# Optimization experiments

Hardware: AMD Instinct MI355X
Metric: run time of the kernel (lower is better)

## Reference

```python
import jax, jax.numpy as jnp
import numpy as np

DIM = 64
D_STATE = 64          # = d_inner // 2, required for consistency
D_CONV = 4
EXPAND = 2
D_INNER = EXPAND * DIM  # 128
BATCH = 2
SEQ = 2048


def setup_inputs() -> dict:
    key = jax.random.key(0)
    k0, k1, k2, k3, k4, k5 = jax.random.split(key, 6)
    return {
        "x": jax.random.normal(k0, (BATCH, SEQ, DIM), jnp.float32),
        # torch nn.Linear weight layout: (out_features, in_features)
        "W_proj": jax.random.normal(k1, (3 * D_INNER, DIM), jnp.float32) / np.sqrt(DIM),
        # torch depthwise Conv1d weight layout: (d_inner, 1, d_conv)
        "conv_w": jax.random.normal(k2, (D_INNER, 1, D_CONV), jnp.float32) / np.sqrt(D_CONV),
        "conv_b": jax.random.normal(k3, (D_INNER,), jnp.float32) * 0.01,
        # negative A so exp(delta * rowsum(A)) is a stable decay (<1)
        "A": -jnp.abs(jax.random.normal(k4, (D_STATE, D_STATE), jnp.float32)) * 0.1,
        "D": jax.random.normal(k5, (D_INNER,), jnp.float32),
    }


def _scan_dir(A_bar, bx, reverse):
    # A_bar, bx: (B, L, n, d). Linear recurrence h_t = A_t * h_{t-1} + bx_t.
    A_t = jnp.moveaxis(A_bar, 1, 0)  # (L, B, n, d)
    b_t = jnp.moveaxis(bx, 1, 0)
    h0 = jnp.zeros(A_t.shape[1:], A_t.dtype)

    def step(h, inp):
        a, b = inp
        h = a * h + b
        return h, h

    _, hs = jax.lax.scan(step, h0, (A_t, b_t), reverse=reverse)
    return jnp.moveaxis(hs, 0, 1)  # (B, L, n, d)


def _forward(x, W_proj, conv_w, conv_b, A, D):
    d_inner = D.shape[0]
    n = A.shape[0]
    k = conv_w.shape[-1]

    xp = x @ W_proj.T                                   # (B, L, 3*d_inner)
    x_c_in, delta_raw, BC = jnp.split(xp, [d_inner, 2 * d_inner], axis=-1)

    # causal depthwise conv1d (torch pads d_conv-1 both sides then slices [:L])
    xc = jnp.swapaxes(x_c_in, 1, 2)                     # (B, d, L)
    xc = jax.lax.conv_general_dilated(
        xc, conv_w, window_strides=(1,), padding=[(k - 1, 0)],
        dimension_numbers=("NCH", "OIH", "NCH"), feature_group_count=d_inner)
    xc = xc + conv_b[None, :, None]
    x_conv = jnp.swapaxes(xc, 1, 2)                     # (B, L, d_inner)

    delta = jax.nn.sigmoid(delta_raw)                   # (B, L, d_inner)
    B_in, C_in = BC[..., :n], BC[..., n:]               # (B, L, n) each

    a = A.sum(axis=1)                                   # 'ij->i' contraction, (n,)
    # A_bar[b,l,n,d] = exp(delta[b,l,d] * a[n])
    A_bar = jnp.exp(delta[:, :, None, :] * a[None, None, :, None])
    # (delta*B) * x, broadcast into (B, L, n, d)
    bx = (delta * x_conv)[:, :, None, :] * B_in[..., None]

    h = _scan_dir(A_bar, bx, False) + _scan_dir(A_bar, bx, True)  # (B,L,n,d)

    y = jnp.einsum("blnd,bln->bld", h, C_in) + D * x_conv
    return y


def reference(x, W_proj, conv_w, conv_b, A, D):
    return _forward(x, W_proj, conv_w, conv_b, A, D)
```

## Files before the change

kernel.cpp:

```cpp
#include <hip/hip_runtime.h>

#define BB   2
#define TT   2048
#define DIN  128
#define NS   64
#define CL   16
#define NC   128
#define NSUP 16
#define SUPW 8
#define NP   32
#define L2E  1.4426950408889634f

typedef float f2_t __attribute__((ext_vector_type(2)));
typedef float f4_t __attribute__((ext_vector_type(4)));

#if __has_builtin(__builtin_amdgcn_exp2f)
__device__ __forceinline__ float fexp2(float x) { return __builtin_amdgcn_exp2f(x); }
#else
__device__ __forceinline__ float fexp2(float x) { return exp2f(x); }
#endif

__device__ __forceinline__ unsigned int f2bfu(float f) {
  unsigned int u = __float_as_uint(f);
  u += 0x7FFFu + ((u >> 16) & 1u);
  return u >> 16;
}
__device__ __forceinline__ unsigned int packbf2(float a, float b) {
  return f2bfu(a) | (f2bfu(b) << 16);
}
__device__ __forceinline__ float bflo(unsigned int u) { return __uint_as_float(u << 16); }
__device__ __forceinline__ float bfhi(unsigned int u) { return __uint_as_float(u & 0xFFFF0000u); }

__global__ __launch_bounds__(128) void k_proj(
    const float* __restrict__ x, const float* __restrict__ W,
    const float* __restrict__ A,
    float* __restrict__ xcin, float* __restrict__ delta,
    float* __restrict__ Bb, float* __restrict__ Cb, float* __restrict__ a2g) {
  __shared__ float xs[128 * 65];
  int tile = blockIdx.x, rg = blockIdx.y, tid = threadIdx.x;
  int base = tile * 128;
  const float4* __restrict__ x4 = (const float4*)(x + (size_t)base * 64);
  for (int i = tid; i < 128 * 16; i += 128) {
    float4 v = x4[i];
    int row = i >> 4, c4 = (i & 15) << 2;
    xs[row * 65 + c4 + 0] = v.x;
    xs[row * 65 + c4 + 1] = v.y;
    xs[row * 65 + c4 + 2] = v.z;
    xs[row * 65 + c4 + 3] = v.w;
  }
  if (tile == 0 && rg == 0 && tid < NS) {
    float s = 0.f;
    for (int m = 0; m < NS; ++m) s += A[tid * NS + m];
    a2g[tid] = s * L2E;
  }
  __syncthreads();
  float xr[64];
#pragma unroll
  for (int k = 0; k < 64; ++k) xr[k] = xs[tid * 65 + k];
  int bt = base + tid;
#pragma unroll 4
  for (int rr = 0; rr < 16; ++rr) {
    int r = rg * 16 + rr;
    const float* __restrict__ wrow = W + r * 64;
    float a0 = 0.f, a1 = 0.f, a2 = 0.f, a3 = 0.f;
#pragma unroll
    for (int k = 0; k < 64; k += 4) {
      a0 = fmaf(xr[k + 0], wrow[k + 0], a0);
      a1 = fmaf(xr[k + 1], wrow[k + 1], a1);
      a2 = fmaf(xr[k + 2], wrow[k + 2], a2);
      a3 = fmaf(xr[k + 3], wrow[k + 3], a3);
    }
    float acc = (a0 + a1) + (a2 + a3);
    if (r < 128) {
      xcin[(size_t)bt * DIN + r] = acc;
    } else if (r < 256) {
      delta[(size_t)bt * DIN + (r - 128)] = 1.f / (1.f + fexp2(-acc * L2E));
    } else if (r < 320) {
      Bb[(size_t)bt * NS + (r - 256)] = acc;
    } else {
      Cb[(size_t)bt * NS + (r - 320)] = acc;
    }
  }
}

__global__ __launch_bounds__(1024) void k_scan1(
    const float* __restrict__ xcin, const float* __restrict__ delta,
    const float* __restrict__ Bb, const float* __restrict__ a2g,
    const float* __restrict__ cw, const float* __restrict__ cb,
    unsigned int* __restrict__ hendP, float* __restrict__ sumd) {
  __shared__ float xcs[(CL + 3) * DIN];
  __shared__ float des[CL * DIN];
  __shared__ float Bs[CL * NS];
  int c = blockIdx.x, b = blockIdx.y;
  int tid = threadIdx.x;
  int d = tid & 127;
  int g = __builtin_amdgcn_readfirstlane(tid >> 7);
  int t0 = c * CL;
  {
    const float* __restrict__ xcB = xcin + (size_t)b * TT * DIN;
    for (int i = tid; i < (CL + 3) * 32; i += 1024) {
      int row = i >> 5, c4 = i & 31;
      int t = t0 - 3 + row;
      float4 v = make_float4(0.f, 0.f, 0.f, 0.f);
      if (t >= 0) v = ((const float4*)(xcB + (size_t)t * DIN))[c4];
      ((float4*)xcs)[i] = v;
    }
    if (tid < CL * 32)
      ((float4*)des)[tid] = ((const float4*)(delta + (size_t)(b * TT + t0) * DIN))[tid];
    if (tid < CL * 16)
      ((float4*)Bs)[tid] = ((const float4*)(Bb + (size_t)(b * TT + t0) * NS))[tid];
  }
  float cw0 = cw[d * 4 + 0], cw1 = cw[d * 4 + 1], cw2 = cw[d * 4 + 2], cw3 = cw[d * 4 + 3];
  float cbd = cb[d];
  int nb = g * 8;
  f2_t a2p[4];
#pragma unroll
  for (int j = 0; j < 4; ++j) { a2p[j].x = a2g[nb + 2 * j]; a2p[j].y = a2g[nb + 2 * j + 1]; }
  __syncthreads();
  f2_t hf[4], hr[4], Pp[4];
#pragma unroll
  for (int j = 0; j < 4; ++j) {
    hf[j] = (f2_t){0.f, 0.f}; hr[j] = (f2_t){0.f, 0.f}; Pp[j] = (f2_t){1.f, 1.f};
  }
  float sd = 0.f;
  float w0 = xcs[0 * DIN + d], w1 = xcs[1 * DIN + d], w2 = xcs[2 * DIN + d];
#pragma unroll
  for (int i = 0; i < CL; ++i) {
    float w3 = xcs[(i + 3) * DIN + d];
    float xconv = fmaf(cw0, w0, fmaf(cw1, w1, fmaf(cw2, w2, fmaf(cw3, w3, cbd))));
    float de = des[i * DIN + d];
    sd += de;
    float dxv = de * xconv;
    const f2_t* __restrict__ B2 = (const f2_t*)&Bs[i * NS + nb];
#pragma unroll
    for (int j = 0; j < 4; ++j) {
      f2_t b2 = dxv * B2[j];
      f2_t e2;
      e2.x = fexp2(de * a2p[j].x);
      e2.y = fexp2(de * a2p[j].y);
      hf[j] = e2 * hf[j] + b2;
      hr[j] = Pp[j] * b2 + hr[j];
      Pp[j] = Pp[j] * e2;
    }
    w0 = w1; w1 = w2; w2 = w3;
  }
  size_t h0 = (((size_t)(0 * NC + c) * BB + b) * NP + (nb >> 1)) * DIN + d;
  size_t h1 = (((size_t)(1 * NC + c) * BB + b) * NP + (nb >> 1)) * DIN + d;
#pragma unroll
  for (int j = 0; j < 4; ++j) {
    hendP[h0 + (size_t)j * DIN] = packbf2(hf[j].x, hf[j].y);
    hendP[h1 + (size_t)j * DIN] = packbf2(hr[j].x, hr[j].y);
  }
  if (g == 0) sumd[(c * BB + b) * DIN + d] = sd;
}

__global__ __launch_bounds__(512) void k_comb(
    const unsigned int* __restrict__ hendP, const float* __restrict__ sumd,
    const float* __restrict__ a2g, unsigned int* __restrict__ hinP) {
  __shared__ float S0[NSUP][64], S1[NSUP][64];
  __shared__ float sdS[NSUP][64];
  __shared__ float C0[NSUP][64], C1[NSUP][64];
  int bid = blockIdx.x;
  int dh = bid & 1;
  int np = (bid >> 1) & 31;
  int dir = (bid >> 6) & 1;
  int b = bid >> 7;
  int tid = threadIdx.x;
  int dl = tid & 63;
  int d = dh * 64 + dl;
  int sl = __builtin_amdgcn_readfirstlane(tid >> 6);
  float a2n0 = a2g[2 * np], a2n1 = a2g[2 * np + 1];
  float hinLo0[2][SUPW], hinLo1[2][SUPW], pfLoc[2][SUPW];
#pragma unroll
  for (int ss = 0; ss < 2; ++ss) {
    int sp = sl + ss * 8;
    float c0 = 0.f, c1 = 0.f, pf = 0.f;
#pragma unroll
    for (int k = 0; k < SUPW; ++k) {
      int cc = sp * SUPW + (dir ? (SUPW - 1 - k) : k);
      float sdv = sumd[(cc * BB + b) * DIN + d];
      unsigned int hv = hendP[(((size_t)(dir * NC + cc) * BB + b) * NP + np) * DIN + d];
      hinLo0[ss][k] = c0; hinLo1[ss][k] = c1; pfLoc[ss][k] = pf;
      float e0 = fexp2(a2n0 * sdv);
      float e1 = fexp2(a2n1 * sdv);
      c0 = fmaf(e0, c0, bflo(hv));
      c1 = fmaf(e1, c1, bfhi(hv));
      pf += sdv;
    }
    S0[sp][dl] = c0; S1[sp][dl] = c1; sdS[sp][dl] = pf;
  }
  __syncthreads();
  if (sl == 0) {
    float c0 = 0.f, c1 = 0.f;
#pragma unroll
    for (int k = 0; k < NSUP; ++k) {
      int sp = dir ? (NSUP - 1 - k) : k;
      C0[sp][dl] = c0; C1[sp][dl] = c1;
      float sv = sdS[sp][dl];
      float e0 = fexp2(a2n0 * sv);
      float e1 = fexp2(a2n1 * sv);
      c0 = fmaf(e0, c0, S0[sp][dl]);
      c1 = fmaf(e1, c1, S1[sp][dl]);
    }
  }
  __syncthreads();
#pragma unroll
  for (int ss = 0; ss < 2; ++ss) {
    int sp = sl + ss * 8;
    float cs0 = C0[sp][dl], cs1 = C1[sp][dl];
#pragma unroll
    for (int k = 0; k < SUPW; ++k) {
      int cc = sp * SUPW + (dir ? (SUPW - 1 - k) : k);
      float pe0 = fexp2(a2n0 * pfLoc[ss][k]);
      float pe1 = fexp2(a2n1 * pfLoc[ss][k]);
      float v0 = fmaf(pe0, cs0, hinLo0[ss][k]);
      float v1 = fmaf(pe1, cs1, hinLo1[ss][k]);
      hinP[(((size_t)(dir * NC + cc) * BB + b) * NP + np) * DIN + d] = packbf2(v0, v1);
    }
  }
}

__global__ __launch_bounds__(1024) void k_scan2(
    const float* __restrict__ xcin, const float* __restrict__ delta,
    const float* __restrict__ Bb, const float* __restrict__ Cb,
    const float* __restrict__ a2g, const float* __restrict__ cw,
    const float* __restrict__ cb, const float* __restrict__ Dp,
    const unsigned int* __restrict__ hinP,
    float* __restrict__ out) {
  __shared__ float yred[8][CL][DIN];
  int c = blockIdx.x, b = blockIdx.y;
  int tid = threadIdx.x;
  int d = tid & 127;
  int g = __builtin_amdgcn_readfirstlane(tid >> 7);
  int dir = g >> 2;
  int nb = (g & 3) * 16;
  float cw0 = cw[d * 4 + 0], cw1 = cw[d * 4 + 1], cw2 = cw[d * 4 + 2], cw3 = cw[d * 4 + 3];
  float cbd = cb[d];
  float Dd = Dp[d];
  f2_t a2p[8];
#pragma unroll
  for (int j = 0; j < 8; ++j) { a2p[j].x = a2g[nb + 2 * j]; a2p[j].y = a2g[nb + 2 * j + 1]; }
  f2_t h2[8];
  size_t hb0 = (((size_t)(dir * NC + c) * BB + b) * NP + (nb >> 1)) * DIN + d;
#pragma unroll
  for (int jp = 0; jp < 8; ++jp) {
    unsigned int u = hinP[hb0 + (size_t)jp * DIN];
    h2[jp].x = bflo(u);
    h2[jp].y = bfhi(u);
  }
  int t0 = c * CL;
  const float* __restrict__ xcB = xcin + (size_t)b * TT * DIN + d;
  const float* __restrict__ deB = delta + (size_t)b * TT * DIN + d;
  const float* __restrict__ BbB = Bb + (size_t)b * TT * NS + nb;
  const float* __restrict__ CbB = Cb + (size_t)b * TT * NS + nb;
  bool addD = (g == 0);
  float w0, w1, w2, w3;
  if (dir == 0) {
    int t = t0;
    w0 = (t - 3 >= 0) ? xcB[(t - 3) * DIN] : 0.f;
    w1 = (t - 2 >= 0) ? xcB[(t - 2) * DIN] : 0.f;
    w2 = (t - 1 >= 0) ? xcB[(t - 1) * DIN] : 0.f;
    w3 = xcB[t * DIN];
#pragma unroll
    for (int i = 0; i < CL; ++i) {
      float xconv = fmaf(cw0, w0, fmaf(cw1, w1, fmaf(cw2, w2, fmaf(cw3, w3, cbd))));
      float de = deB[t * DIN];
      float dxv = de * xconv;
      f2_t y2 = (f2_t){0.f, 0.f};
#pragma unroll
      for (int jq = 0; jq < 4; ++jq) {
        f4_t bq = *(const f4_t*)&BbB[t * NS + jq * 4];
        f4_t cq = *(const f4_t*)&CbB[t * NS + jq * 4];
        f2_t blo = __builtin_shufflevector(bq, bq, 0, 1);
        f2_t bhi = __builtin_shufflevector(bq, bq, 2, 3);
        f2_t clo = __builtin_shufflevector(cq, cq, 0, 1);
        f2_t chi = __builtin_shufflevector(cq, cq, 2, 3);
        int jp = 2 * jq;
        f2_t e2;
        e2.x = fexp2(de * a2p[jp].x);
        e2.y = fexp2(de * a2p[jp].y);
        h2[jp] = e2 * h2[jp] + dxv * blo;
        y2 = h2[jp] * clo + y2;
        f2_t e3;
        e3.x = fexp2(de * a2p[jp + 1].x);
        e3.y = fexp2(de * a2p[jp + 1].y);
        h2[jp + 1] = e3 * h2[jp + 1] + dxv * bhi;
        y2 = h2[jp + 1] * chi + y2;
      }
      float yv = y2.x + y2.y;
      if (addD) yv = fmaf(Dd, xconv, yv);
      yred[g][i][d] = yv;
      if (i < CL - 1) { ++t; w0 = w1; w1 = w2; w2 = w3; w3 = xcB[t * DIN]; }
    }
  } else {
    int t = t0 + CL - 1;
    w3 = xcB[t * DIN];
    w2 = xcB[(t - 1) * DIN];
    w1 = xcB[(t - 2) * DIN];
    w0 = xcB[(t - 3) * DIN];
#pragma unroll
    for (int i = 0; i < CL; ++i) {
      float xconv = fmaf(cw0, w0, fmaf(cw1, w1, fmaf(cw2, w2, fmaf(cw3, w3, cbd))));
      float de = deB[t * DIN];
      float dxv = de * xconv;
      f2_t y2 = (f2_t){0.f, 0.f};
#pragma unroll
      for (int jq = 0; jq < 4; ++jq) {
        f4_t bq = *(const f4_t*)&BbB[t * NS + jq * 4];
        f4_t cq = *(const f4_t*)&CbB[t * NS + jq * 4];
        f2_t blo = __builtin_shufflevector(bq, bq, 0, 1);
        f2_t bhi = __builtin_shufflevector(bq, bq, 2, 3);
        f2_t clo = __builtin_shufflevector(cq, cq, 0, 1);
        f2_t chi = __builtin_shufflevector(cq, cq, 2, 3);
        int jp = 2 * jq;
        f2_t e2;
        e2.x = fexp2(de * a2p[jp].x);
        e2.y = fexp2(de * a2p[jp].y);
        h2[jp] = e2 * h2[jp] + dxv * blo;
        y2 = h2[jp] * clo + y2;
        f2_t e3;
        e3.x = fexp2(de * a2p[jp + 1].x);
        e3.y = fexp2(de * a2p[jp + 1].y);
        h2[jp + 1] = e3 * h2[jp + 1] + dxv * bhi;
        y2 = h2[jp + 1] * chi + y2;
      }
      float yv = y2.x + y2.y;
      yred[g][i][d] = yv;
      if (i < CL - 1) { --t; w3 = w2; w2 = w1; w1 = w0; w0 = (t - 3 >= 0) ? xcB[(t - 3) * DIN] : 0.f; }
    }
  }
  __syncthreads();
#pragma unroll
  for (int k = 0; k < 2; ++k) {
    int p = k * 1024 + tid;
    int i = p >> 7, d2 = p & 127;
    int ir = CL - 1 - i;
    float sf = (yred[0][i][d2] + yred[1][i][d2]) + (yred[2][i][d2] + yred[3][i][d2]);
    float sr = (yred[4][ir][d2] + yred[5][ir][d2]) + (yred[6][ir][d2] + yred[7][ir][d2]);
    out[((size_t)b * TT + t0 + i) * DIN + d2] = sf + sr;
  }
}

extern "C" void kernel_launch(void* const* d_in, const int* in_sizes, int n_in,
                              void* d_out, int out_size, void* d_ws, size_t ws_size,
                              hipStream_t stream) {
  const float* x  = (const float*)d_in[0];
  const float* W  = (const float*)d_in[1];
  const float* cw = (const float*)d_in[2];
  const float* cb = (const float*)d_in[3];
  const float* A  = (const float*)d_in[4];
  const float* Dp = (const float*)d_in[5];
  float* out = (float*)d_out;

  float* ws = (float*)d_ws;
  float* xcin   = ws;
  float* delta  = xcin + 524288;
  float* Bbuf   = delta + 524288;
  float* Cbuf   = Bbuf + 262144;
  float* a2g    = Cbuf + 262144;
  float* sumd   = a2g + 128;
  unsigned int* hendP = (unsigned int*)(sumd + 32768);
  unsigned int* hinP  = hendP + 2097152;

  hipLaunchKernelGGL(k_proj,  dim3(32, 24), dim3(128), 0, stream,
                     x, W, A, xcin, delta, Bbuf, Cbuf, a2g);
  hipLaunchKernelGGL(k_scan1, dim3(NC, BB), dim3(1024), 0, stream,
                     xcin, delta, Bbuf, a2g, cw, cb, hendP, sumd);
  hipLaunchKernelGGL(k_comb,  dim3(256), dim3(512), 0, stream,
                     hendP, sumd, a2g, hinP);
  hipLaunchKernelGGL(k_scan2, dim3(NC, BB), dim3(1024), 0, stream,
                     xcin, delta, Bbuf, Cbuf, a2g, cw, cb, Dp, hinP, out);
}
```

Before: 57.11 us.

## Fuse scan1, combine and scan2 into one cooperative kernel with grid syncs

Merges the three scan-phase kernels into a single cooperative launch of 256 blocks of 1024 threads, separating the phases with grid.sync(). The combine phase is remapped onto 1024 threads per block, so each thread now handles one super-chunk instead of two. The aim is to remove two kernel launch boundaries and their drain/refill gaps. In exchange it adds grid-wide barrier cost, larger combined LDS use that may limit residency, and the requirement that all 256 blocks are co-resident.

```diff
diff --git a/kernel.cpp b/kernel.cpp
--- a/kernel.cpp
+++ b/kernel.cpp
@@ -1,4 +1,6 @@
 #include <hip/hip_runtime.h>
+#include <hip/hip_cooperative_groups.h>
+namespace cg = cooperative_groups;
 
 #define BB   2
 #define TT   2048
@@ -83,104 +85,105 @@
   }
 }
 
-__global__ __launch_bounds__(1024) void k_scan1(
+__global__ __launch_bounds__(1024) void k_main(
     const float* __restrict__ xcin, const float* __restrict__ delta,
-    const float* __restrict__ Bb, const float* __restrict__ a2g,
-    const float* __restrict__ cw, const float* __restrict__ cb,
-    unsigned int* __restrict__ hendP, float* __restrict__ sumd) {
+    const float* __restrict__ Bb, const float* __restrict__ Cb,
+    const float* __restrict__ a2g, const float* __restrict__ cw,
+    const float* __restrict__ cb, const float* __restrict__ Dp,
+    unsigned int* __restrict__ hendP, float* __restrict__ sumd,
+    unsigned int* __restrict__ hinP, float* __restrict__ out) {
   __shared__ float xcs[(CL + 3) * DIN];
   __shared__ float des[CL * DIN];
   __shared__ float Bs[CL * NS];
-  int c = blockIdx.x, b = blockIdx.y;
-  int tid = threadIdx.x;
-  int d = tid & 127;
-  int g = __builtin_amdgcn_readfirstlane(tid >> 7);
-  int t0 = c * CL;
-  {
-    const float* __restrict__ xcB = xcin + (size_t)b * TT * DIN;
-    for (int i = tid; i < (CL + 3) * 32; i += 1024) {
-      int row = i >> 5, c4 = i & 31;
-      int t = t0 - 3 + row;
-      float4 v = make_float4(0.f, 0.f, 0.f, 0.f);
-      if (t >= 0) v = ((const float4*)(xcB + (size_t)t * DIN))[c4];
-      ((float4*)xcs)[i] = v;
-    }
-    if (tid < CL * 32)
-      ((float4*)des)[tid] = ((const float4*)(delta + (size_t)(b * TT + t0) * DIN))[tid];
-    if (tid < CL * 16)
-      ((float4*)Bs)[tid] = ((const float4*)(Bb + (size_t)(b * TT + t0) * NS))[tid];
-  }
+  __shared__ float S0[NSUP][64], S1[NSUP][64], sdS[NSUP][64];
+  __shared__ float C0[NSUP][64], C1[NSUP][64];
+  __shared__ float yred[8][CL][DIN];
+  cg::grid_group grid = cg::this_grid();
+  const int bid = blockIdx.x, tid = threadIdx.x;
+  const int d = tid & 127;
+
   float cw0 = cw[d * 4 + 0], cw1 = cw[d * 4 + 1], cw2 = cw[d * 4 + 2], cw3 = cw[d * 4 + 3];
   float cbd = cb[d];
-  int nb = g * 8;
-  f2_t a2p[4];
-#pragma unroll
-  for (int j = 0; j < 4; ++j) { a2p[j].x = a2g[nb + 2 * j]; a2p[j].y = a2g[nb + 2 * j + 1]; }
-  __syncthreads();
-  f2_t hf[4], hr[4], Pp[4];
-#pragma unroll
-  for (int j = 0; j < 4; ++j) {
-    hf[j] = (f2_t){0.f, 0.f}; hr[j] = (f2_t){0.f, 0.f}; Pp[j] = (f2_t){1.f, 1.f};
-  }
-  float sd = 0.f;
-  float w0 = xcs[0 * DIN + d], w1 = xcs[1 * DIN + d], w2 = xcs[2 * DIN + d];
-#pragma unroll
-  for (int i = 0; i < CL; ++i) {
-    float w3 = xcs[(i + 3) * DIN + d];
-    float xconv = fmaf(cw0, w0, fmaf(cw1, w1, fmaf(cw2, w2, fmaf(cw3, w3, cbd))));
-    float de = des[i * DIN + d];
-    sd += de;
-    float dxv = de * xconv;
-    const f2_t* __restrict__ B2 = (const f2_t*)&Bs[i * NS + nb];
+  float Dd = Dp[d];
+
+  {
+    int c = bid & 127, b = bid >> 7;
+    int g = __builtin_amdgcn_readfirstlane(tid >> 7);
+    int t0 = c * CL;
+    {
+      const float* __restrict__ xcB = xcin + (size_t)b * TT * DIN;
+      for (int i = tid; i < (CL + 3) * 32; i += 1024) {
+        int row = i >> 5, c4 = i & 31;
+        int t = t0 - 3 + row;
+        float4 v = make_float4(0.f, 0.f, 0.f, 0.f);
+        if (t >= 0) v = ((const float4*)(xcB + (size_t)t * DIN))[c4];
+        ((float4*)xcs)[i] = v;
+      }
+      if (tid < CL * 32)
+        ((float4*)des)[tid] = ((const float4*)(delta + (size_t)(b * TT + t0) * DIN))[tid];
+      if (tid < CL * 16)
+        ((float4*)Bs)[tid] = ((const float4*)(Bb + (size_t)(b * TT + t0) * NS))[tid];
+    }
+    int nb = g * 8;
+    f2_t a2p[4];
+#pragma unroll
+    for (int j = 0; j < 4; ++j) { a2p[j].x = a2g[nb + 2 * j]; a2p[j].y = a2g[nb + 2 * j + 1]; }
+    __syncthreads();
+    f2_t hf[4], hr[4], Pp[4];
 #pragma unroll
     for (int j = 0; j < 4; ++j) {
-      f2_t b2 = dxv * B2[j];
-      f2_t e2;
-      e2.x = fexp2(de * a2p[j].x);
-      e2.y = fexp2(de * a2p[j].y);
-      hf[j] = e2 * hf[j] + b2;
-      hr[j] = Pp[j] * b2 + hr[j];
-      Pp[j] = Pp[j] * e2;
-    }
-    w0 = w1; w1 = w2; w2 = w3;
-  }
-  size_t h0 = (((size_t)(0 * NC + c) * BB + b) * NP + (nb >> 1)) * DIN + d;
-  size_t h1 = (((size_t)(1 * NC + c) * BB + b) * NP + (nb >> 1)) * DIN + d;
-#pragma unroll
-  for (int j = 0; j < 4; ++j) {
-    hendP[h0 + (size_t)j * DIN] = packbf2(hf[j].x, hf[j].y);
-    hendP[h1 + (size_t)j * DIN] = packbf2(hr[j].x, hr[j].y);
-  }
-  if (g == 0) sumd[(c * BB + b) * DIN + d] = sd;
-}
-
-__global__ __launch_bounds__(512) void k_comb(
-    const unsigned int* __restrict__ hendP, const float* __restrict__ sumd,
-    const float* __restrict__ a2g, unsigned int* __restrict__ hinP) {
-  __shared__ float S0[NSUP][64], S1[NSUP][64];
-  __shared__ float sdS[NSUP][64];
-  __shared__ float C0[NSUP][64], C1[NSUP][64];
-  int bid = blockIdx.x;
-  int dh = bid & 1;
-  int np = (bid >> 1) & 31;
-  int dir = (bid >> 6) & 1;
-  int b = bid >> 7;
-  int tid = threadIdx.x;
-  int dl = tid & 63;
-  int d = dh * 64 + dl;
-  int sl = __builtin_amdgcn_readfirstlane(tid >> 6);
-  float a2n0 = a2g[2 * np], a2n1 = a2g[2 * np + 1];
-  float hinLo0[2][SUPW], hinLo1[2][SUPW], pfLoc[2][SUPW];
-#pragma unroll
-  for (int ss = 0; ss < 2; ++ss) {
-    int sp = sl + ss * 8;
+      hf[j] = (f2_t){0.f, 0.f}; hr[j] = (f2_t){0.f, 0.f}; Pp[j] = (f2_t){1.f, 1.f};
+    }
+    float sd = 0.f;
+    float w0 = xcs[0 * DIN + d], w1 = xcs[1 * DIN + d], w2 = xcs[2 * DIN + d];
+#pragma unroll
+    for (int i = 0; i < CL; ++i) {
+      float w3 = xcs[(i + 3) * DIN + d];
+      float xconv = fmaf(cw0, w0, fmaf(cw1, w1, fmaf(cw2, w2, fmaf(cw3, w3, cbd))));
+      float de = des[i * DIN + d];
+      sd += de;
+      float dxv = de * xconv;
+      const f2_t* __restrict__ B2 = (const f2_t*)&Bs[i * NS + nb];
+#pragma unroll
+      for (int j = 0; j < 4; ++j) {
+        f2_t b2 = dxv * B2[j];
+        f2_t e2;
+        e2.x = fexp2(de * a2p[j].x);
+        e2.y = fexp2(de * a2p[j].y);
+        hf[j] = e2 * hf[j] + b2;
+        hr[j] = Pp[j] * b2 + hr[j];
+        Pp[j] = Pp[j] * e2;
+      }
+      w0 = w1; w1 = w2; w2 = w3;
+    }
+    size_t h0 = (((size_t)(0 * NC + c) * BB + b) * NP + (nb >> 1)) * DIN + d;
+    size_t h1 = (((size_t)(1 * NC + c) * BB + b) * NP + (nb >> 1)) * DIN + d;
+#pragma unroll
+    for (int j = 0; j < 4; ++j) {
+      hendP[h0 + (size_t)j * DIN] = packbf2(hf[j].x, hf[j].y);
+      hendP[h1 + (size_t)j * DIN] = packbf2(hr[j].x, hr[j].y);
+    }
+    if (g == 0) sumd[(c * BB + b) * DIN + d] = sd;
+  }
+  grid.sync();
+
+  {
+    int dh = bid & 1;
+    int np = (bid >> 1) & 31;
+    int dir = (bid >> 6) & 1;
+    int b = bid >> 7;
+    int dl = tid & 63;
+    int dd = dh * 64 + dl;
+    int sp = __builtin_amdgcn_readfirstlane(tid >> 6);
+    float a2n0 = a2g[2 * np], a2n1 = a2g[2 * np + 1];
+    float hinLo0[SUPW], hinLo1[SUPW], pfLoc[SUPW];
     float c0 = 0.f, c1 = 0.f, pf = 0.f;
 #pragma unroll
     for (int k = 0; k < SUPW; ++k) {
       int cc = sp * SUPW + (dir ? (SUPW - 1 - k) : k);
-      float sdv = sumd[(cc * BB + b) * DIN + d];
-      unsigned int hv = hendP[(((size_t)(dir * NC + cc) * BB + b) * NP + np) * DIN + d];
-      hinLo0[ss][k] = c0; hinLo1[ss][k] = c1; pfLoc[ss][k] = pf;
+      float sdv = sumd[(cc * BB + b) * DIN + dd];
+      unsigned int hv = hendP[(((size_t)(dir * NC + cc) * BB + b) * NP + np) * DIN + dd];
+      hinLo0[k] = c0; hinLo1[k] = c1; pfLoc[k] = pf;
       float e0 = fexp2(a2n0 * sdv);
       float e1 = fexp2(a2n1 * sdv);
       c0 = fmaf(e0, c0, bflo(hv));
@@ -188,156 +191,141 @@
       pf += sdv;
     }
     S0[sp][dl] = c0; S1[sp][dl] = c1; sdS[sp][dl] = pf;
-  }
-  __syncthreads();
-  if (sl == 0) {
-    float c0 = 0.f, c1 = 0.f;
-#pragma unroll
-    for (int k = 0; k < NSUP; ++k) {
-      int sp = dir ? (NSUP - 1 - k) : k;
-      C0[sp][dl] = c0; C1[sp][dl] = c1;
-      float sv = sdS[sp][dl];
-      float e0 = fexp2(a2n0 * sv);
-      float e1 = fexp2(a2n1 * sv);
-      c0 = fmaf(e0, c0, S0[sp][dl]);
-      c1 = fmaf(e1, c1, S1[sp][dl]);
-    }
-  }
-  __syncthreads();
-#pragma unroll
-  for (int ss = 0; ss < 2; ++ss) {
-    int sp = sl + ss * 8;
+    __syncthreads();
+    if (sp == 0) {
+      float g0 = 0.f, g1 = 0.f;
+#pragma unroll
+      for (int k = 0; k < NSUP; ++k) {
+        int spp = dir ? (NSUP - 1 - k) : k;
+        C0[spp][dl] = g0; C1[spp][dl] = g1;
+        float sv = sdS[spp][dl];
+        float e0 = fexp2(a2n0 * sv);
+        float e1 = fexp2(a2n1 * sv);
+        g0 = fmaf(e0, g0, S0[spp][dl]);
+        g1 = fmaf(e1, g1, S1[spp][dl]);
+      }
+    }
+    __syncthreads();
     float cs0 = C0[sp][dl], cs1 = C1[sp][dl];
 #pragma unroll
     for (int k = 0; k < SUPW; ++k) {
       int cc = sp * SUPW + (dir ? (SUPW - 1 - k) : k);
-      float pe0 = fexp2(a2n0 * pfLoc[ss][k]);
-      float pe1 = fexp2(a2n1 * pfLoc[ss][k]);
-      float v0 = fmaf(pe0, cs0, hinLo0[ss][k]);
-      float v1 = fmaf(pe1, cs1, hinLo1[ss][k]);
-      hinP[(((size_t)(dir * NC + cc) * BB + b) * NP + np) * DIN + d] = packbf2(v0, v1);
-    }
-  }
-}
-
-__global__ __launch_bounds__(1024) void k_scan2(
-    const float* __restrict__ xcin, const float* __restrict__ delta,
-    const float* __restrict__ Bb, const float* __restrict__ Cb,
-    const float* __restrict__ a2g, const float* __restrict__ cw,
-    const float* __restrict__ cb, const float* __restrict__ Dp,
-    const unsigned int* __restrict__ hinP,
-    float* __restrict__ out) {
-  __shared__ float yred[8][CL][DIN];
-  int c = blockIdx.x, b = blockIdx.y;
-  int tid = threadIdx.x;
-  int d = tid & 127;
-  int g = __builtin_amdgcn_readfirstlane(tid >> 7);
-  int dir = g >> 2;
-  int nb = (g & 3) * 16;
-  float cw0 = cw[d * 4 + 0], cw1 = cw[d * 4 + 1], cw2 = cw[d * 4 + 2], cw3 = cw[d * 4 + 3];
-  float cbd = cb[d];
-  float Dd = Dp[d];
-  f2_t a2p[8];
-#pragma unroll
-  for (int j = 0; j < 8; ++j) { a2p[j].x = a2g[nb + 2 * j]; a2p[j].y = a2g[nb + 2 * j + 1]; }
-  f2_t h2[8];
-  size_t hb0 = (((size_t)(dir * NC + c) * BB + b) * NP + (nb >> 1)) * DIN + d;
-#pragma unroll
-  for (int jp = 0; jp < 8; ++jp) {
-    unsigned int u = hinP[hb0 + (size_t)jp * DIN];
-    h2[jp].x = bflo(u);
-    h2[jp].y = bfhi(u);
-  }
-  int t0 = c * CL;
-  const float* __restrict__ xcB = xcin + (size_t)b * TT * DIN + d;
-  const float* __restrict__ deB = delta + (size_t)b * TT * DIN + d;
-  const float* __restrict__ BbB = Bb + (size_t)b * TT * NS + nb;
-  const float* __restrict__ CbB = Cb + (size_t)b * TT * NS + nb;
-  bool addD = (g == 0);
-  float w0, w1, w2, w3;
-  if (dir == 0) {
-    int t = t0;
-    w0 = (t - 3 >= 0) ? xcB[(t - 3) * DIN] : 0.f;
-    w1 = (t - 2 >= 0) ? xcB[(t - 2) * DIN] : 0.f;
-    w2 = (t - 1 >= 0) ? xcB[(t - 1) * DIN] : 0.f;
-    w3 = xcB[t * DIN];
-#pragma unroll
-    for (int i = 0; i < CL; ++i) {
-      float xconv = fmaf(cw0, w0, fmaf(cw1, w1, fmaf(cw2, w2, fmaf(cw3, w3, cbd))));
-      float de = deB[t * DIN];
-      float dxv = de * xconv;
-      f2_t y2 = (f2_t){0.f, 0.f};
-#pragma unroll
-      for (int jq = 0; jq < 4; ++jq) {
-        f4_t bq = *(const f4_t*)&BbB[t * NS + jq * 4];
-        f4_t cq = *(const f4_t*)&CbB[t * NS + jq * 4];
-        f2_t blo = __builtin_shufflevector(bq, bq, 0, 1);
-        f2_t bhi = __builtin_shufflevector(bq, bq, 2, 3);
-        f2_t clo = __builtin_shufflevector(cq, cq, 0, 1);
-        f2_t chi = __builtin_shufflevector(cq, cq, 2, 3);
-        int jp = 2 * jq;
-        f2_t e2;
-        e2.x = fexp2(de * a2p[jp].x);
-        e2.y = fexp2(de * a2p[jp].y);
-        h2[jp] = e2 * h2[jp] + dxv * blo;
-        y2 = h2[jp] * clo + y2;
-        f2_t e3;
-        e3.x = fexp2(de * a2p[jp + 1].x);
-        e3.y = fexp2(de * a2p[jp + 1].y);
-        h2[jp + 1] = e3 * h2[jp + 1] + dxv * bhi;
-        y2 = h2[jp + 1] * chi + y2;
-      }
-      float yv = y2.x + y2.y;
-      if (addD) yv = fmaf(Dd, xconv, yv);
-      yred[g][i][d] = yv;
-      if (i < CL - 1) { ++t; w0 = w1; w1 = w2; w2 = w3; w3 = xcB[t * DIN]; }
-    }
-  } else {
-    int t = t0 + CL - 1;
-    w3 = xcB[t * DIN];
-    w2 = xcB[(t - 1) * DIN];
-    w1 = xcB[(t - 2) * DIN];
-    w0 = xcB[(t - 3) * DIN];
-#pragma unroll
-    for (int i = 0; i < CL; ++i) {
-      float xconv = fmaf(cw0, w0, fmaf(cw1, w1, fmaf(cw2, w2, fmaf(cw3, w3, cbd))));
-      float de = deB[t * DIN];
-      float dxv = de * xconv;
-      f2_t y2 = (f2_t){0.f, 0.f};
-#pragma unroll
-      for (int jq = 0; jq < 4; ++jq) {
-        f4_t bq = *(const f4_t*)&BbB[t * NS + jq * 4];
-        f4_t cq = *(const f4_t*)&CbB[t * NS + jq * 4];
-        f2_t blo = __builtin_shufflevector(bq, bq, 0, 1);
-        f2_t bhi = __builtin_shufflevector(bq, bq, 2, 3);
-        f2_t clo = __builtin_shufflevector(cq, cq, 0, 1);
-        f2_t chi = __builtin_shufflevector(cq, cq, 2, 3);
-        int jp = 2 * jq;
-        f2_t e2;
-        e2.x = fexp2(de * a2p[jp].x);
-        e2.y = fexp2(de * a2p[jp].y);
-        h2[jp] = e2 * h2[jp] + dxv * blo;
-        y2 = h2[jp] * clo + y2;
-        f2_t e3;
-        e3.x = fexp2(de * a2p[jp + 1].x);
-        e3.y = fexp2(de * a2p[jp + 1].y);
-        h2[jp + 1] = e3 * h2[jp + 1] + dxv * bhi;
-        y2 = h2[jp + 1] * chi + y2;
-      }
-      float yv = y2.x + y2.y;
-      yred[g][i][d] = yv;
-      if (i < CL - 1) { --t; w3 = w2; w2 = w1; w1 = w0; w0 = (t - 3 >= 0) ? xcB[(t - 3) * DIN] : 0.f; }
-    }
-  }
-  __syncthreads();
-#pragma unroll
-  for (int k = 0; k < 2; ++k) {
-    int p = k * 1024 + tid;
-    int i = p >> 7, d2 = p & 127;
-    int ir = CL - 1 - i;
-    float sf = (yred[0][i][d2] + yred[1][i][d2]) + (yred[2][i][d2] + yred[3][i][d2]);
-    float sr = (yred[4][ir][d2] + yred[5][ir][d2]) + (yred[6][ir][d2] + yred[7][ir][d2]);
-    out[((size_t)b * TT + t0 + i) * DIN + d2] = sf + sr;
+      float pe0 = fexp2(a2n0 * pfLoc[k]);
+      float pe1 = fexp2(a2n1 * pfLoc[k]);
+      float v0 = fmaf(pe0, cs0, hinLo0[k]);
+      float v1 = fmaf(pe1, cs1, hinLo1[k]);
+      hinP[(((size_t)(dir * NC + cc) * BB + b) * NP + np) * DIN + dd] = packbf2(v0, v1);
+    }
+  }
+  grid.sync();
+
+  {
+    int c = bid & 127, b = bid >> 7;
+    int g = __builtin_amdgcn_readfirstlane(tid >> 7);
+    int dir = g >> 2;
+    int nb = (g & 3) * 16;
+    f2_t a2p[8];
+#pragma unroll
+    for (int j = 0; j < 8; ++j) { a2p[j].x = a2g[nb + 2 * j]; a2p[j].y = a2g[nb + 2 * j + 1]; }
+    f2_t h2[8];
+    size_t hb0 = (((size_t)(dir * NC + c) * BB + b) * NP + (nb >> 1)) * DIN + d;
+#pragma unroll
+    for (int jp = 0; jp < 8; ++jp) {
+      unsigned int u = hinP[hb0 + (size_t)jp * DIN];
+      h2[jp].x = bflo(u);
+      h2[jp].y = bfhi(u);
+    }
+    int t0 = c * CL;
+    const float* __restrict__ xcB = xcin + (size_t)b * TT * DIN + d;
+    const float* __restrict__ deB = delta + (size_t)b * TT * DIN + d;
+    const float* __restrict__ BbB = Bb + (size_t)b * TT * NS + nb;
+    const float* __restrict__ CbB = Cb + (size_t)b * TT * NS + nb;
+    bool addD = (g == 0);
+    float w0, w1, w2, w3;
+    if (dir == 0) {
+      int t = t0;
+      w0 = (t - 3 >= 0) ? xcB[(t - 3) * DIN] : 0.f;
+      w1 = (t - 2 >= 0) ? xcB[(t - 2) * DIN] : 0.f;
+      w2 = (t - 1 >= 0) ? xcB[(t - 1) * DIN] : 0.f;
+      w3 = xcB[t * DIN];
+#pragma unroll
+      for (int i = 0; i < CL; ++i) {
+        float xconv = fmaf(cw0, w0, fmaf(cw1, w1, fmaf(cw2, w2, fmaf(cw3, w3, cbd))));
+        float de = deB[t * DIN];
+        float dxv = de * xconv;
+        f2_t y2 = (f2_t){0.f, 0.f};
+#pragma unroll
+        for (int jq = 0; jq < 4; ++jq) {
+          f4_t bq = *(const f4_t*)&BbB[t * NS + jq * 4];
+          f4_t cq = *(const f4_t*)&CbB[t * NS + jq * 4];
+          f2_t blo = __builtin_shufflevector(bq, bq, 0, 1);
+          f2_t bhi = __builtin_shufflevector(bq, bq, 2, 3);
+          f2_t clo = __builtin_shufflevector(cq, cq, 0, 1);
+          f2_t chi = __builtin_shufflevector(cq, cq, 2, 3);
+          int jp = 2 * jq;
+          f2_t e2;
+          e2.x = fexp2(de * a2p[jp].x);
+          e2.y = fexp2(de * a2p[jp].y);
+          h2[jp] = e2 * h2[jp] + dxv * blo;
+          y2 = h2[jp] * clo + y2;
+          f2_t e3;
+          e3.x = fexp2(de * a2p[jp + 1].x);
+          e3.y = fexp2(de * a2p[jp + 1].y);
+          h2[jp + 1] = e3 * h2[jp + 1] + dxv * bhi;
+          y2 = h2[jp + 1] * chi + y2;
+        }
+        float yv = y2.x + y2.y;
+        if (addD) yv = fmaf(Dd, xconv, yv);
+        yred[g][i][d] = yv;
+        if (i < CL - 1) { ++t; w0 = w1; w1 = w2; w2 = w3; w3 = xcB[t * DIN]; }
+      }
+    } else {
+      int t = t0 + CL - 1;
+      w3 = xcB[t * DIN];
+      w2 = xcB[(t - 1) * DIN];
+      w1 = xcB[(t - 2) * DIN];
+      w0 = xcB[(t - 3) * DIN];
+#pragma unroll
+      for (int i = 0; i < CL; ++i) {
+        float xconv = fmaf(cw0, w0, fmaf(cw1, w1, fmaf(cw2, w2, fmaf(cw3, w3, cbd))));
+        float de = deB[t * DIN];
+        float dxv = de * xconv;
+        f2_t y2 = (f2_t){0.f, 0.f};
+#pragma unroll
+        for (int jq = 0; jq < 4; ++jq) {
+          f4_t bq = *(const f4_t*)&BbB[t * NS + jq * 4];
+          f4_t cq = *(const f4_t*)&CbB[t * NS + jq * 4];
+          f2_t blo = __builtin_shufflevector(bq, bq, 0, 1);
+          f2_t bhi = __builtin_shufflevector(bq, bq, 2, 3);
+          f2_t clo = __builtin_shufflevector(cq, cq, 0, 1);
+          f2_t chi = __builtin_shufflevector(cq, cq, 2, 3);
+          int jp = 2 * jq;
+          f2_t e2;
+          e2.x = fexp2(de * a2p[jp].x);
+          e2.y = fexp2(de * a2p[jp].y);
+          h2[jp] = e2 * h2[jp] + dxv * blo;
+          y2 = h2[jp] * clo + y2;
+          f2_t e3;
+          e3.x = fexp2(de * a2p[jp + 1].x);
+          e3.y = fexp2(de * a2p[jp + 1].y);
+          h2[jp + 1] = e3 * h2[jp + 1] + dxv * bhi;
+          y2 = h2[jp + 1] * chi + y2;
+        }
+        float yv = y2.x + y2.y;
+        yred[g][i][d] = yv;
+        if (i < CL - 1) { --t; w3 = w2; w2 = w1; w1 = w0; w0 = (t - 3 >= 0) ? xcB[(t - 3) * DIN] : 0.f; }
+      }
+    }
+    __syncthreads();
+#pragma unroll
+    for (int k = 0; k < 2; ++k) {
+      int p = k * 1024 + tid;
+      int i = p >> 7, d2 = p & 127;
+      int ir = CL - 1 - i;
+      float sf = (yred[0][i][d2] + yred[1][i][d2]) + (yred[2][i][d2] + yred[3][i][d2]);
+      float sr = (yred[4][ir][d2] + yred[5][ir][d2]) + (yred[6][ir][d2] + yred[7][ir][d2]);
+      out[((size_t)b * TT + t0 + i) * DIN + d2] = sf + sr;
+    }
   }
 }
 
@@ -362,12 +350,13 @@
   unsigned int* hendP = (unsigned int*)(sumd + 32768);
   unsigned int* hinP  = hendP + 2097152;
 
-  hipLaunchKernelGGL(k_proj,  dim3(32, 24), dim3(128), 0, stream,
+  hipLaunchKernelGGL(k_proj, dim3(32, 24), dim3(128), 0, stream,
                      x, W, A, xcin, delta, Bbuf, Cbuf, a2g);
-  hipLaunchKernelGGL(k_scan1, dim3(NC, BB), dim3(1024), 0, stream,
-                     xcin, delta, Bbuf, a2g, cw, cb, hendP, sumd);
-  hipLaunchKernelGGL(k_comb,  dim3(256), dim3(512), 0, stream,
-                     hendP, sumd, a2g, hinP);
-  hipLaunchKernelGGL(k_scan2, dim3(NC, BB), dim3(1024), 0, stream,
-                     xcin, delta, Bbuf, Cbuf, a2g, cw, cb, Dp, hinP, out);
-}
+
+  void* kargs[] = {
+    (void*)&xcin, (void*)&delta, (void*)&Bbuf, (void*)&Cbuf, (void*)&a2g,
+    (void*)&cw, (void*)&cb, (void*)&Dp,
+    (void*)&hendP, (void*)&sumd, (void*)&hinP, (void*)&out
+  };
+  hipLaunchCooperativeKernel((void*)k_main, dim3(256), dim3(1024), kargs, 0, stream);
+}
```

Measured after the change: 119.2 us. 109% more time.

## Fuse input projection into first scan kernel and recompute A row sums locally

Applied to the files above, without the earlier changes.

Removes the separate projection kernel. Each scan1 block now computes the projection for its own chunk of 16 timesteps plus a 3-row conv halo, writing the results to shared memory for the local scan and to global memory for later kernels. Each kernel also recomputes the A row sums itself instead of reading a shared a2g buffer. This drops one launch and the global round trip for scan1's inputs, at the cost of redundant halo projection work, W rows read from global by every block, and repeated A sums.

```diff
diff --git a/kernel.cpp b/kernel.cpp
--- a/kernel.cpp
+++ b/kernel.cpp
@@ -31,92 +31,81 @@
 __device__ __forceinline__ float bflo(unsigned int u) { return __uint_as_float(u << 16); }
 __device__ __forceinline__ float bfhi(unsigned int u) { return __uint_as_float(u & 0xFFFF0000u); }
 
-__global__ __launch_bounds__(128) void k_proj(
+__global__ __launch_bounds__(1024) void k_scan1p(
     const float* __restrict__ x, const float* __restrict__ W,
     const float* __restrict__ A,
+    const float* __restrict__ cw, const float* __restrict__ cb,
     float* __restrict__ xcin, float* __restrict__ delta,
-    float* __restrict__ Bb, float* __restrict__ Cb, float* __restrict__ a2g) {
-  __shared__ float xs[128 * 65];
-  int tile = blockIdx.x, rg = blockIdx.y, tid = threadIdx.x;
-  int base = tile * 128;
-  const float4* __restrict__ x4 = (const float4*)(x + (size_t)base * 64);
-  for (int i = tid; i < 128 * 16; i += 128) {
-    float4 v = x4[i];
-    int row = i >> 4, c4 = (i & 15) << 2;
-    xs[row * 65 + c4 + 0] = v.x;
-    xs[row * 65 + c4 + 1] = v.y;
-    xs[row * 65 + c4 + 2] = v.z;
-    xs[row * 65 + c4 + 3] = v.w;
-  }
-  if (tile == 0 && rg == 0 && tid < NS) {
-    float s = 0.f;
-    for (int m = 0; m < NS; ++m) s += A[tid * NS + m];
-    a2g[tid] = s * L2E;
-  }
-  __syncthreads();
-  float xr[64];
-#pragma unroll
-  for (int k = 0; k < 64; ++k) xr[k] = xs[tid * 65 + k];
-  int bt = base + tid;
-#pragma unroll 4
-  for (int rr = 0; rr < 16; ++rr) {
-    int r = rg * 16 + rr;
-    const float* __restrict__ wrow = W + r * 64;
-    float a0 = 0.f, a1 = 0.f, a2 = 0.f, a3 = 0.f;
-#pragma unroll
-    for (int k = 0; k < 64; k += 4) {
-      a0 = fmaf(xr[k + 0], wrow[k + 0], a0);
-      a1 = fmaf(xr[k + 1], wrow[k + 1], a1);
-      a2 = fmaf(xr[k + 2], wrow[k + 2], a2);
-      a3 = fmaf(xr[k + 3], wrow[k + 3], a3);
-    }
-    float acc = (a0 + a1) + (a2 + a3);
-    if (r < 128) {
-      xcin[(size_t)bt * DIN + r] = acc;
-    } else if (r < 256) {
-      delta[(size_t)bt * DIN + (r - 128)] = 1.f / (1.f + fexp2(-acc * L2E));
-    } else if (r < 320) {
-      Bb[(size_t)bt * NS + (r - 256)] = acc;
-    } else {
-      Cb[(size_t)bt * NS + (r - 320)] = acc;
-    }
-  }
-}
-
-__global__ __launch_bounds__(1024) void k_scan1(
-    const float* __restrict__ xcin, const float* __restrict__ delta,
-    const float* __restrict__ Bb, const float* __restrict__ a2g,
-    const float* __restrict__ cw, const float* __restrict__ cb,
+    float* __restrict__ Bb, float* __restrict__ Cb,
     unsigned int* __restrict__ hendP, float* __restrict__ sumd) {
+  __shared__ float xs[19 * 64];
+  __shared__ float a2s[NS];
   __shared__ float xcs[(CL + 3) * DIN];
   __shared__ float des[CL * DIN];
   __shared__ float Bs[CL * NS];
+  __shared__ float Cs[CL * NS];
   int c = blockIdx.x, b = blockIdx.y;
   int tid = threadIdx.x;
   int d = tid & 127;
   int g = __builtin_amdgcn_readfirstlane(tid >> 7);
   int t0 = c * CL;
-  {
-    const float* __restrict__ xcB = xcin + (size_t)b * TT * DIN;
-    for (int i = tid; i < (CL + 3) * 32; i += 1024) {
-      int row = i >> 5, c4 = i & 31;
-      int t = t0 - 3 + row;
-      float4 v = make_float4(0.f, 0.f, 0.f, 0.f);
-      if (t >= 0) v = ((const float4*)(xcB + (size_t)t * DIN))[c4];
-      ((float4*)xcs)[i] = v;
-    }
-    if (tid < CL * 32)
-      ((float4*)des)[tid] = ((const float4*)(delta + (size_t)(b * TT + t0) * DIN))[tid];
-    if (tid < CL * 16)
-      ((float4*)Bs)[tid] = ((const float4*)(Bb + (size_t)(b * TT + t0) * NS))[tid];
+  for (int i = tid; i < 19 * 16; i += 1024) {
+    int row = i >> 4;
+    int t = t0 - 3 + row;
+    float4 v = make_float4(0.f, 0.f, 0.f, 0.f);
+    if (t >= 0) v = ((const float4*)(x + ((size_t)b * TT + t) * 64))[i & 15];
+    ((float4*)xs)[i] = v;
+  }
+  if (tid < NS) {
+    float s = 0.f;
+    const float* __restrict__ Ar = A + tid * NS;
+#pragma unroll 8
+    for (int m = 0; m < NS; ++m) s += Ar[m];
+    a2s[tid] = s * L2E;
+  }
+  __syncthreads();
+  for (int i = tid; i < 6528; i += 1024) {
+    int kind, row, col, wr;
+    if (i < 2432)      { kind = 0; row = i >> 7;            col = i & 127; wr = col; }
+    else if (i < 4480) { kind = 1; row = (i - 2432) >> 7;   col = (i - 2432) & 127; wr = 128 + col; }
+    else if (i < 5504) { kind = 2; row = (i - 4480) >> 6;   col = (i - 4480) & 63;  wr = 256 + col; }
+    else               { kind = 3; row = (i - 5504) >> 6;   col = (i - 5504) & 63;  wr = 320 + col; }
+    int xrow = (kind == 0) ? row : (row + 3);
+    const float4* __restrict__ w4 = (const float4*)(W + wr * 64);
+    const float4* __restrict__ x4r = (const float4*)(xs + xrow * 64);
+    float a0 = 0.f, a1 = 0.f, a2 = 0.f, a3 = 0.f;
+#pragma unroll
+    for (int k = 0; k < 16; ++k) {
+      float4 wv = w4[k];
+      float4 xv = x4r[k];
+      a0 = fmaf(wv.x, xv.x, a0);
+      a1 = fmaf(wv.y, xv.y, a1);
+      a2 = fmaf(wv.z, xv.z, a2);
+      a3 = fmaf(wv.w, xv.w, a3);
+    }
+    float acc = (a0 + a1) + (a2 + a3);
+    if (kind == 0) {
+      xcs[row * DIN + col] = acc;
+      if (row >= 3) xcin[((size_t)b * TT + (t0 + row - 3)) * DIN + col] = acc;
+    } else if (kind == 1) {
+      float dv = 1.f / (1.f + fexp2(-acc * L2E));
+      des[row * DIN + col] = dv;
+      delta[((size_t)b * TT + (t0 + row)) * DIN + col] = dv;
+    } else if (kind == 2) {
+      Bs[row * NS + col] = acc;
+      Bb[((size_t)b * TT + (t0 + row)) * NS + col] = acc;
+    } else {
+      Cs[row * NS + col] = acc;
+      Cb[((size_t)b * TT + (t0 + row)) * NS + col] = acc;
+    }
   }
   float cw0 = cw[d * 4 + 0], cw1 = cw[d * 4 + 1], cw2 = cw[d * 4 + 2], cw3 = cw[d * 4 + 3];
   float cbd = cb[d];
   int nb = g * 8;
+  __syncthreads();
   f2_t a2p[4];
 #pragma unroll
-  for (int j = 0; j < 4; ++j) { a2p[j].x = a2g[nb + 2 * j]; a2p[j].y = a2g[nb + 2 * j + 1]; }
-  __syncthreads();
+  for (int j = 0; j < 4; ++j) { a2p[j].x = a2s[nb + 2 * j]; a2p[j].y = a2s[nb + 2 * j + 1]; }
   f2_t hf[4], hr[4], Pp[4];
 #pragma unroll
   for (int j = 0; j < 4; ++j) {
@@ -156,10 +145,11 @@
 
 __global__ __launch_bounds__(512) void k_comb(
     const unsigned int* __restrict__ hendP, const float* __restrict__ sumd,
-    const float* __restrict__ a2g, unsigned int* __restrict__ hinP) {
+    const float* __restrict__ A, unsigned int* __restrict__ hinP) {
   __shared__ float S0[NSUP][64], S1[NSUP][64];
   __shared__ float sdS[NSUP][64];
   __shared__ float C0[NSUP][64], C1[NSUP][64];
+  __shared__ float sc2[2];
   int bid = blockIdx.x;
   int dh = bid & 1;
   int np = (bid >> 1) & 31;
@@ -169,7 +159,15 @@
   int dl = tid & 63;
   int d = dh * 64 + dl;
   int sl = __builtin_amdgcn_readfirstlane(tid >> 6);
-  float a2n0 = a2g[2 * np], a2n1 = a2g[2 * np + 1];
+  if (tid < 2) {
+    float s = 0.f;
+    const float* __restrict__ Ar = A + (2 * np + tid) * NS;
+#pragma unroll 8
+    for (int m = 0; m < NS; ++m) s += Ar[m];
+    sc2[tid] = s * L2E;
+  }
+  __syncthreads();
+  float a2n0 = sc2[0], a2n1 = sc2[1];
   float hinLo0[2][SUPW], hinLo1[2][SUPW], pfLoc[2][SUPW];
 #pragma unroll
   for (int ss = 0; ss < 2; ++ss) {
@@ -223,23 +221,32 @@
 __global__ __launch_bounds__(1024) void k_scan2(
     const float* __restrict__ xcin, const float* __restrict__ delta,
     const float* __restrict__ Bb, const float* __restrict__ Cb,
-    const float* __restrict__ a2g, const float* __restrict__ cw,
+    const float* __restrict__ A, const float* __restrict__ cw,
     const float* __restrict__ cb, const float* __restrict__ Dp,
     const unsigned int* __restrict__ hinP,
     float* __restrict__ out) {
   __shared__ float yred[8][CL][DIN];
+  __shared__ float a2s[NS];
   int c = blockIdx.x, b = blockIdx.y;
   int tid = threadIdx.x;
   int d = tid & 127;
   int g = __builtin_amdgcn_readfirstlane(tid >> 7);
   int dir = g >> 2;
   int nb = (g & 3) * 16;
+  if (tid < NS) {
+    float s = 0.f;
+    const float* __restrict__ Ar = A + tid * NS;
+#pragma unroll 8
+    for (int m = 0; m < NS; ++m) s += Ar[m];
+    a2s[tid] = s * L2E;
+  }
+  __syncthreads();
   float cw0 = cw[d * 4 + 0], cw1 = cw[d * 4 + 1], cw2 = cw[d * 4 + 2], cw3 = cw[d * 4 + 3];
   float cbd = cb[d];
   float Dd = Dp[d];
   f2_t a2p[8];
 #pragma unroll
-  for (int j = 0; j < 8; ++j) { a2p[j].x = a2g[nb + 2 * j]; a2p[j].y = a2g[nb + 2 * j + 1]; }
+  for (int j = 0; j < 8; ++j) { a2p[j].x = a2s[nb + 2 * j]; a2p[j].y = a2s[nb + 2 * j + 1]; }
   f2_t h2[8];
   size_t hb0 = (((size_t)(dir * NC + c) * BB + b) * NP + (nb >> 1)) * DIN + d;
 #pragma unroll
@@ -357,17 +364,14 @@
   float* delta  = xcin + 524288;
   float* Bbuf   = delta + 524288;
   float* Cbuf   = Bbuf + 262144;
-  float* a2g    = Cbuf + 262144;
-  float* sumd   = a2g + 128;
+  float* sumd   = Cbuf + 262144;
   unsigned int* hendP = (unsigned int*)(sumd + 32768);
   unsigned int* hinP  = hendP + 2097152;
 
-  hipLaunchKernelGGL(k_proj,  dim3(32, 24), dim3(128), 0, stream,
-                     x, W, A, xcin, delta, Bbuf, Cbuf, a2g);
-  hipLaunchKernelGGL(k_scan1, dim3(NC, BB), dim3(1024), 0, stream,
-                     xcin, delta, Bbuf, a2g, cw, cb, hendP, sumd);
-  hipLaunchKernelGGL(k_comb,  dim3(256), dim3(512), 0, stream,
-                     hendP, sumd, a2g, hinP);
-  hipLaunchKernelGGL(k_scan2, dim3(NC, BB), dim3(1024), 0, stream,
-                     xcin, delta, Bbuf, Cbuf, a2g, cw, cb, Dp, hinP, out);
-}
+  hipLaunchKernelGGL(k_scan1p, dim3(NC, BB), dim3(1024), 0, stream,
+                     x, W, A, cw, cb, xcin, delta, Bbuf, Cbuf, hendP, sumd);
+  hipLaunchKernelGGL(k_comb,   dim3(256), dim3(512), 0, stream,
+                     hendP, sumd, A, hinP);
+  hipLaunchKernelGGL(k_scan2,  dim3(NC, BB), dim3(1024), 0, stream,
+                     xcin, delta, Bbuf, Cbuf, A, cw, cb, Dp, hinP, out);
+}
```

Measured after the change: 85.48 us. 1.5x slower.
